# Kernel tuning notes

Hardware: AMD Instinct MI355X
Metric: run time of the kernel (lower is better)

The kernel has to match this reference:

```python
import jax, jax.numpy as jnp
import numpy as np

B, S, H, V, E = 64, 20, 128, 50257, 300


def gru(p, x, h):
    # tf.contrib.rnn.GRUCell: r,u = sigmoid([x,h]@Wg + bg); c = tanh([x, r*h]@Wc + bc); h' = u*h + (1-u)*c
    gk, gb, ck, cb = p
    xh = jnp.concatenate([x, h], axis=-1)
    r, u = jnp.split(jax.nn.sigmoid(xh @ gk + gb), 2, axis=-1)
    c = jnp.tanh(jnp.concatenate([x, r * h], axis=-1) @ ck + cb)
    return u * h + (1.0 - u) * c


def setup_inputs() -> dict:
    key = jax.random.key(0)
    ks = jax.random.split(key, 32)
    s = 0.08
    rn = lambda k, shp: (jax.random.normal(k, shp, jnp.float32) * s)
    inp = {}
    inp['x'] = jax.random.randint(ks[0], (B, S), 0, V, dtype=jnp.int32)
    inp['x_length'] = jax.random.randint(ks[1], (B,), 1, S + 1, dtype=jnp.int32)
    inp['y'] = jax.random.randint(ks[2], (B, S), 0, V, dtype=jnp.int32)
    inp['y_length'] = jax.random.randint(ks[3], (B,), 1, S + 1, dtype=jnp.int32)
    inp['embedding'] = jax.random.normal(ks[4], (V, E), jnp.float32) * 0.1
    # encoder GRU: layer0 in=E, layer1 in=H
    inp['e0_gk'] = rn(ks[5], (E + H, 2 * H)); inp['e0_gb'] = rn(ks[6], (2 * H,))
    inp['e0_ck'] = rn(ks[7], (E + H, H));     inp['e0_cb'] = rn(ks[8], (H,))
    inp['e1_gk'] = rn(ks[9], (2 * H, 2 * H)); inp['e1_gb'] = rn(ks[10], (2 * H,))
    inp['e1_ck'] = rn(ks[11], (2 * H, H));    inp['e1_cb'] = rn(ks[12], (H,))
    # decoder GRU: layer0 in = E + attention_size(H) = E+H, layer1 in=H
    inp['d0_gk'] = rn(ks[13], (E + 2 * H, 2 * H)); inp['d0_gb'] = rn(ks[14], (2 * H,))
    inp['d0_ck'] = rn(ks[15], (E + 2 * H, H));     inp['d0_cb'] = rn(ks[16], (H,))
    inp['d1_gk'] = rn(ks[17], (2 * H, 2 * H));     inp['d1_gb'] = rn(ks[18], (2 * H,))
    inp['d1_ck'] = rn(ks[19], (2 * H, H));         inp['d1_cb'] = rn(ks[20], (H,))
    # Bahdanau attention (num_units=H) + attention output layer + vocab projection
    inp['W_mem'] = rn(ks[21], (H, H))
    inp['W_q'] = rn(ks[22], (H, H))
    inp['v_att'] = rn(ks[23], (H,))
    inp['W_attn'] = rn(ks[24], (2 * H, H))
    inp['W_proj'] = rn(ks[25], (H, V))
    inp['b_proj'] = jnp.zeros((V,), jnp.float32)
    return inp


def _forward(x, x_length, y, y_length, embedding,
             e0_gk, e0_gb, e0_ck, e0_cb, e1_gk, e1_gb, e1_ck, e1_cb,
             d0_gk, d0_gb, d0_ck, d0_cb, d1_gk, d1_gb, d1_ck, d1_cb,
             W_mem, W_q, v_att, W_attn, W_proj, b_proj):
    e0 = (e0_gk, e0_gb, e0_ck, e0_cb)
    e1 = (e1_gk, e1_gb, e1_ck, e1_cb)
    d0 = (d0_gk, d0_gb, d0_ck, d0_cb)
    d1 = (d1_gk, d1_gb, d1_ck, d1_cb)
    t_idx = jnp.arange(S)
    x_valid = t_idx[None, :] < x_length[:, None]   # [B,S]
    y_valid = t_idx[None, :] < y_length[:, None]   # [B,S]

    # ---- encoder: 2-layer GRU dynamic_rnn with sequence_length semantics ----
    ex = embedding[x]                               # [B,S,E]
    zeros = jnp.zeros((x.shape[0], H), embedding.dtype)

    def enc_step(carry, inp_t):
        h0, h1 = carry
        xt, vt = inp_t                              # xt [B,E], vt [B,1]
        n0 = gru(e0, xt, h0)
        n1 = gru(e1, n0, h1)
        n0 = jnp.where(vt, n0, h0)                  # copy-through past seq end
        n1 = jnp.where(vt, n1, h1)
        return (n0, n1), jnp.where(vt, n1, 0.0)     # outputs zeroed past seq end

    (h0f, h1f), mem = jax.lax.scan(
        enc_step, (zeros, zeros),
        (ex.transpose(1, 0, 2), x_valid.T[:, :, None]))
    memory = mem.transpose(1, 0, 2)                 # [B,S,H] encoder outputs

    # ---- Bahdanau attention precompute ----
    keys = jnp.einsum('bsh,hu->bsu', memory, W_mem)  # memory_layer(memory)
    neg_inf = jnp.finfo(memory.dtype).min

    # ---- attention decoder (TrainingHelper) ----
    ey = embedding[y]                               # [B,S,E]
    attn0 = jnp.zeros((x.shape[0], H), embedding.dtype)

    def dec_step(carry, inp_t):
        h0, h1, attn = carry
        yt, vt = inp_t                              # yt [B,E], vt [B,1]
        ci = jnp.concatenate([yt, attn], axis=-1)   # cell input = [emb, prev attention]
        n0 = gru(d0, ci, h0)
        n1 = gru(d1, n0, h1)
        q = n1 @ W_q                                # query_layer(cell_output)
        sc = jnp.einsum('bsu,u->bs', jnp.tanh(keys + q[:, None, :]), v_att)
        sc = jnp.where(x_valid, sc, neg_inf)        # memory_sequence_length mask
        al = jax.nn.softmax(sc, axis=-1)            # [B,S]
        ctx = jnp.einsum('bs,bsh->bh', al, memory)  # context
        na = jnp.concatenate([n1, ctx], axis=-1) @ W_attn  # attention_layer (no bias)
        logits = na @ W_proj + b_proj               # projection_layer
        logits = jnp.where(vt, logits, 0.0)         # dynamic_decode zeroes finished emits
        return (n0, n1, na), logits

    _, logits = jax.lax.scan(
        dec_step, (h0f, h1f, attn0),
        (ey.transpose(1, 0, 2), y_valid.T[:, :, None]))
    return logits.transpose(1, 0, 2)                # [B,S,V] rnn_output


def reference(x, x_length, y, y_length, embedding,
              e0_gk, e0_gb, e0_ck, e0_cb, e1_gk, e1_gb, e1_ck, e1_cb,
              d0_gk, d0_gb, d0_ck, d0_cb, d1_gk, d1_gb, d1_ck, d1_cb,
              W_mem, W_q, v_att, W_attn, W_proj, b_proj):
    return _forward(x, x_length, y, y_length, embedding,
                    e0_gk, e0_gb, e0_ck, e0_cb, e1_gk, e1_gb, e1_ck, e1_cb,
                    d0_gk, d0_gb, d0_ck, d0_cb, d1_gk, d1_gb, d1_ck, d1_cb,
                    W_mem, W_q, v_att, W_attn, W_proj, b_proj)
```

## Files before the change

kernel.cpp:

```cpp
#include <hip/hip_runtime.h>
#include <hip/hip_bf16.h>

#define Bb 64
#define Ss 20
#define Hh 128
#define Vv 50257
#define Ee 300
#define Vpad 50304

typedef short bf16x8 __attribute__((ext_vector_type(8)));
typedef float f32x4 __attribute__((ext_vector_type(4)));

__device__ __forceinline__ unsigned short f2bf(float f){
  unsigned u = __float_as_uint(f);
  u += 0x7fff + ((u >> 16) & 1);
  return (unsigned short)(u >> 16);
}
__device__ __forceinline__ float sigm(float x){ return 1.f / (1.f + __expf(-x)); }
__device__ __forceinline__ float tanh_fast(float x){
  float e = __expf(2.f * x);
  return 1.f - 2.f / (e + 1.f);
}

template<int K4>
__device__ __forceinline__ float dotT(const float* __restrict__ w, const float* v){
  float a0 = 0.f, a1 = 0.f, a2 = 0.f, a3 = 0.f;
  const float4* w4 = (const float4*)w;
  const float4* v4 = (const float4*)v;
#pragma unroll
  for (int i = 0; i < K4; i++){
    float4 wv = w4[i]; float4 xv = v4[i];
    a0 = fmaf(wv.x, xv.x, a0); a1 = fmaf(wv.y, xv.y, a1);
    a2 = fmaf(wv.z, xv.z, a2); a3 = fmaf(wv.w, xv.w, a3);
  }
  return (a0 + a1) + (a2 + a3);
}


struct TMat { const float* src; float* dst; int r0, R, C; };
struct TList { TMat m[15]; };

__global__ __launch_bounds__(256) void wtrans_kernel(TList L){
  TMat t = L.m[blockIdx.y];
  int idx = blockIdx.x * 256 + threadIdx.x;
  int total = t.R * t.C;
  if (idx >= total) return;
  int o = idx / t.R;
  int i = idx - o * t.R;
  t.dst[idx] = t.src[(size_t)(t.r0 + i) * t.C + o];
}

__global__ __launch_bounds__(256) void wpt_kernel(const float* __restrict__ Wp,
                                                  unsigned short* __restrict__ Wpt){
  __shared__ unsigned short tile[64][136];
  int n0 = blockIdx.x * 64;
  int tid = threadIdx.x;
  for (int idx = tid; idx < 8192; idx += 256){
    int k = idx >> 6, nn = idx & 63;
    int n = n0 + nn;
    float f = (n < Vv) ? Wp[(size_t)k * Vv + n] : 0.f;
    tile[nn][k] = f2bf(f);
  }
  __syncthreads();
  for (int idx = tid; idx < 1024; idx += 256){
    int nn = idx >> 4, c = idx & 15;
    uint4 v = *reinterpret_cast<const uint4*>(&tile[nn][c * 8]);
    *reinterpret_cast<uint4*>(Wpt + (((size_t)(n0 + nn)) << 7) + c * 8) = v;
  }
}


__global__ __launch_bounds__(256) void pre_kernel(
    const int* __restrict__ x, const int* __restrict__ y, const float* __restrict__ emb,
    const float* __restrict__ egx, const float* __restrict__ ecx,
    const float* __restrict__ egb, const float* __restrict__ ecb,
    const float* __restrict__ dgx, const float* __restrict__ dcx,
    const float* __restrict__ dgb, const float* __restrict__ dcb,
    float* __restrict__ epg, float* __restrict__ epc,
    float* __restrict__ dpg, float* __restrict__ dpc)
{
  __shared__ __align__(16) float er[Ee];
  int tid = threadIdx.x, ti = blockIdx.x, which = blockIdx.y;
  int tok = which ? y[ti] : x[ti];
  if (tid < 75)
    ((float4*)er)[tid] = ((const float4*)(emb + (size_t)tok * Ee))[tid];
  __syncthreads();
  const float* gx = which ? dgx : egx;
  const float* cx = which ? dcx : ecx;
  float accg = (which ? dgb : egb)[tid] + dotT<75>(gx + (size_t)tid * Ee, er);
  (which ? dpg : epg)[ti * 256 + tid] = accg;
  if (tid < 128){
    float accc = (which ? dcb : ecb)[tid] + dotT<75>(cx + (size_t)tid * Ee, er);
    (which ? dpc : epc)[ti * 128 + tid] = accc;
  }
}


__global__ __launch_bounds__(256, 1) void recur2(
    const int* __restrict__ xlen,
    const float* __restrict__ epg, const float* __restrict__ epc,
    const float* __restrict__ dpg, const float* __restrict__ dpc,
    const float* __restrict__ e0_gh_t, const float* __restrict__ e0_ch_t,
    const float* __restrict__ e1_g_t, const float* __restrict__ e1_c_t,
    const float* __restrict__ e1_gb,  const float* __restrict__ e1_cb,
    const float* __restrict__ d0_gah_t, const float* __restrict__ d0_cah_t,
    const float* __restrict__ d1_g_t, const float* __restrict__ d1_c_t,
    const float* __restrict__ d1_gb,  const float* __restrict__ d1_cb,
    const float* __restrict__ W_mem_t, const float* __restrict__ W_q_t,
    const float* __restrict__ W_attn_t, const float* __restrict__ v_att,
    unsigned short* __restrict__ na_bf)
{
  __shared__ __align__(16) float mem_s[Ss][Hh];
  __shared__ __align__(16) float keys_s[Ss][132];
  __shared__ __align__(16) float h0[Hh], h1[Hh], attn[Hh], n0[Hh], n1[Hh], rh[Hh], q[Hh], ctx[Hh];
  __shared__ __align__(16) float gates[2*Hh];
  __shared__ __align__(16) float vatt_s[Hh];
  __shared__ float part[Ss][8], als[Ss];

  const int tid = threadIdx.x, b = blockIdx.x;
  if (tid < Hh){ h0[tid] = 0.f; h1[tid] = 0.f; attn[tid] = 0.f; vatt_s[tid] = v_att[tid]; }
  __syncthreads();
  const int xl = xlen[b];

  for (int t = 0; t < Ss; t++){
    const int tix = b * Ss + t;
    {
      float g = epg[(tix << 8) + tid] + dotT<32>(e0_gh_t + tid * 128, h0);
      float sg = sigm(g);
      if (tid < Hh) rh[tid] = sg * h0[tid];
      else          gates[tid] = sg;
    }
    __syncthreads();
    {
      int o = tid >> 1, half = tid & 1;
      float a = dotT<16>(e0_ch_t + o * 128 + half * 64, rh + half * 64);
      a += __shfl_xor(a, 1);
      if (!half){
        float c = tanh_fast(epc[(tix << 7) + o] + a);
        float u = gates[128 + o];
        n0[o] = u * h0[o] + (1.f - u) * c;
      }
    }
    __syncthreads();
    {
      float g1 = e1_gb[tid] + dotT<32>(e1_g_t + tid * 256, n0)
                            + dotT<32>(e1_g_t + tid * 256 + 128, h1);
      float sg = sigm(g1);
      if (tid < Hh) rh[tid] = sg * h1[tid];
      else          gates[tid] = sg;
    }
    __syncthreads();
    {
      int o = tid >> 1, half = tid & 1;
      const float* base = e1_c_t + o * 256 + half * 128;
      float a = half ? dotT<32>(base, rh) : dotT<32>(base, n0);
      a += __shfl_xor(a, 1);
      if (!half){
        float c = tanh_fast(e1_cb[o] + a);
        float u = gates[128 + o];
        float nh = u * h1[o] + (1.f - u) * c;
        bool v = (t < xl);
        mem_s[t][o] = v ? nh : 0.f;
        h1[o] = v ? nh : h1[o];
        h0[o] = v ? n0[o] : h0[o];
      }
    }
    __syncthreads();
  }

  for (int idx = tid; idx < Ss * Hh; idx += 256){
    int s = idx >> 7, j = idx & 127;
    keys_s[s][j] = dotT<32>(W_mem_t + j * 128, mem_s[s]);
  }
  __syncthreads();

  for (int t = 0; t < Ss; t++){
    const int tix = b * Ss + t;
    {
      float g = dpg[(tix << 8) + tid] + dotT<32>(d0_gah_t + tid * 256, attn)
                                      + dotT<32>(d0_gah_t + tid * 256 + 128, h0);
      float sg = sigm(g);
      if (tid < Hh) rh[tid] = sg * h0[tid];
      else          gates[tid] = sg;
    }
    __syncthreads();
    {
      int o = tid >> 1, half = tid & 1;
      const float* base = d0_cah_t + o * 256 + half * 128;
      float a = half ? dotT<32>(base, rh) : dotT<32>(base, attn);
      a += __shfl_xor(a, 1);
      if (!half){
        float c = tanh_fast(dpc[(tix << 7) + o] + a);
        float u = gates[128 + o];
        float nv = u * h0[o] + (1.f - u) * c;
        n0[o] = nv; h0[o] = nv;
      }
    }
    __syncthreads();
    {
      float g1 = d1_gb[tid] + dotT<32>(d1_g_t + tid * 256, n0)
                            + dotT<32>(d1_g_t + tid * 256 + 128, h1);
      float sg = sigm(g1);
      if (tid < Hh) rh[tid] = sg * h1[tid];
      else          gates[tid] = sg;
    }
    __syncthreads();
    {
      int o = tid >> 1, half = tid & 1;
      const float* base = d1_c_t + o * 256 + half * 128;
      float a = half ? dotT<32>(base, rh) : dotT<32>(base, n0);
      a += __shfl_xor(a, 1);
      if (!half){
        float c = tanh_fast(d1_cb[o] + a);
        float u = gates[128 + o];
        float nh = u * h1[o] + (1.f - u) * c;
        n1[o] = nh; h1[o] = nh;
      }
    }
    __syncthreads();
    {
      int o = tid >> 1, half = tid & 1;
      float a = dotT<16>(W_q_t + o * 128 + half * 64, n1 + half * 64);
      a += __shfl_xor(a, 1);
      if (!half) q[o] = a;
    }
    __syncthreads();
    if (tid < Ss * 8){
      int s = tid >> 3, p = tid & 7;
      float a = 0.f;
#pragma unroll
      for (int c2 = 0; c2 < 16; c2++){
        int u2 = p * 16 + c2;
        a += tanh_fast(keys_s[s][u2] + q[u2]) * vatt_s[u2];
      }
      part[s][p] = a;
    }
    __syncthreads();
    if (tid < 64){
      int s = tid;
      bool valid = (s < Ss) && (s < xl);
      float sc = -3.4e38f;
      if (valid){ sc = 0.f;
#pragma unroll
        for (int p = 0; p < 8; p++) sc += part[s][p];
      }
      float mx = sc;
#pragma unroll
      for (int off = 32; off >= 1; off >>= 1) mx = fmaxf(mx, __shfl_xor(mx, off));
      float e = valid ? __expf(sc - mx) : 0.f;
      float sm = e;
#pragma unroll
      for (int off = 32; off >= 1; off >>= 1) sm += __shfl_xor(sm, off);
      if (s < Ss) als[s] = e / sm;
    }
    __syncthreads();
    if (tid < Hh){
      float a = 0.f;
#pragma unroll
      for (int s = 0; s < Ss; s++) a += als[s] * mem_s[s][tid];
      ctx[tid] = a;
    }
    __syncthreads();
    {
      int o = tid >> 1, half = tid & 1;
      const float* base = W_attn_t + o * 256 + half * 128;
      float a = half ? dotT<32>(base, ctx) : dotT<32>(base, n1);
      a += __shfl_xor(a, 1);
      if (!half){
        attn[o] = a;
        na_bf[(tix << 7) + o] = f2bf(a);
      }
    }
    __syncthreads();
  }
}


__global__ __launch_bounds__(256) void proj2(
    const unsigned short* __restrict__ na_bf, const unsigned short* __restrict__ Wpt,
    const float* __restrict__ b_proj, const int* __restrict__ ylen,
    float* __restrict__ out)
{
  __shared__ int yl_s[Bb];
  const int tid = threadIdx.x;
  if (tid < Bb) yl_s[tid] = ylen[tid];
  const int n0 = blockIdx.x * 128, m0 = blockIdx.y * 64;
  const int lane = tid & 63, w = tid >> 6, lm = lane & 15, qq = lane >> 4;

  f32x4 acc[4][2];
#pragma unroll
  for (int mt = 0; mt < 4; mt++){ acc[mt][0] = (f32x4){0,0,0,0}; acc[mt][1] = (f32x4){0,0,0,0}; }

#pragma unroll
  for (int ks = 0; ks < 4; ks++){
    int ko = ks * 32 + qq * 8;
    bf16x8 b0 = *(const bf16x8*)(Wpt + (((size_t)(n0 + w*32 + lm)) << 7) + ko);
    bf16x8 b1 = *(const bf16x8*)(Wpt + (((size_t)(n0 + w*32 + 16 + lm)) << 7) + ko);
#pragma unroll
    for (int mt = 0; mt < 4; mt++){
      bf16x8 a = *(const bf16x8*)(na_bf + (((size_t)(m0 + mt*16 + lm)) << 7) + ko);
      acc[mt][0] = __builtin_amdgcn_mfma_f32_16x16x32_bf16(a, b0, acc[mt][0], 0, 0, 0);
      acc[mt][1] = __builtin_amdgcn_mfma_f32_16x16x32_bf16(a, b1, acc[mt][1], 0, 0, 0);
    }
  }
  __syncthreads();

#pragma unroll
  for (int mt = 0; mt < 4; mt++){
    int row = m0 + mt*16 + qq*4;
#pragma unroll
    for (int n2 = 0; n2 < 2; n2++){
      int col = n0 + w*32 + n2*16 + lm;
      if (col < Vv){
        float bp = b_proj[col];
#pragma unroll
        for (int r = 0; r < 4; r++){
          int rr = row + r;
          int bb = rr / Ss;
          int tt = rr - bb * Ss;
          float val = (tt < yl_s[bb]) ? (acc[mt][n2][r] + bp) : 0.f;
          out[(size_t)rr * Vv + col] = val;
        }
      }
    }
  }
}

extern "C" void kernel_launch(void* const* d_in, const int* in_sizes, int n_in,
                              void* d_out, int out_size, void* d_ws, size_t ws_size,
                              hipStream_t stream) {
  const int*   x        = (const int*)d_in[0];
  const int*   x_length = (const int*)d_in[1];
  const int*   y        = (const int*)d_in[2];
  const int*   y_length = (const int*)d_in[3];
  const float* emb      = (const float*)d_in[4];
  const float* e0_gk = (const float*)d_in[5];  const float* e0_gb = (const float*)d_in[6];
  const float* e0_ck = (const float*)d_in[7];  const float* e0_cb = (const float*)d_in[8];
  const float* e1_gk = (const float*)d_in[9];  const float* e1_gb = (const float*)d_in[10];
  const float* e1_ck = (const float*)d_in[11]; const float* e1_cb = (const float*)d_in[12];
  const float* d0_gk = (const float*)d_in[13]; const float* d0_gb = (const float*)d_in[14];
  const float* d0_ck = (const float*)d_in[15]; const float* d0_cb = (const float*)d_in[16];
  const float* d1_gk = (const float*)d_in[17]; const float* d1_gb = (const float*)d_in[18];
  const float* d1_ck = (const float*)d_in[19]; const float* d1_cb = (const float*)d_in[20];
  const float* W_mem = (const float*)d_in[21]; const float* W_q   = (const float*)d_in[22];
  const float* v_att = (const float*)d_in[23]; const float* W_attn= (const float*)d_in[24];
  const float* W_proj= (const float*)d_in[25]; const float* b_proj= (const float*)d_in[26];
  float* out = (float*)d_out;

  size_t off = 0;
  auto alloc = [&](size_t bytes) -> void* {
    void* p = (char*)d_ws + off;
    off += (bytes + 255) & ~(size_t)255;
    return p;
  };
  unsigned short* Wpt   = (unsigned short*)alloc((size_t)Vpad * 128 * 2);
  unsigned short* na_bf = (unsigned short*)alloc((size_t)Bb * Ss * Hh * 2);
  float* epg = (float*)alloc((size_t)Bb*Ss*256*4);
  float* epc = (float*)alloc((size_t)Bb*Ss*128*4);
  float* dpg = (float*)alloc((size_t)Bb*Ss*256*4);
  float* dpc = (float*)alloc((size_t)Bb*Ss*128*4);
  float* e0_gx_t  = (float*)alloc(256*300*4);
  float* e0_gh_t  = (float*)alloc(256*128*4);
  float* e0_cx_t  = (float*)alloc(128*300*4);
  float* e0_ch_t  = (float*)alloc(128*128*4);
  float* e1_g_t   = (float*)alloc(256*256*4);
  float* e1_c_t   = (float*)alloc(128*256*4);
  float* d0_gx_t  = (float*)alloc(256*300*4);
  float* d0_gah_t = (float*)alloc(256*256*4);
  float* d0_cx_t  = (float*)alloc(128*300*4);
  float* d0_cah_t = (float*)alloc(128*256*4);
  float* d1_g_t   = (float*)alloc(256*256*4);
  float* d1_c_t   = (float*)alloc(128*256*4);
  float* W_mem_t  = (float*)alloc(128*128*4);
  float* W_q_t    = (float*)alloc(128*128*4);
  float* W_attn_t = (float*)alloc(128*256*4);

  TList L;
  L.m[0]  = { e0_gk, e0_gx_t,    0, 300, 256 };
  L.m[1]  = { e0_gk, e0_gh_t,  300, 128, 256 };
  L.m[2]  = { e0_ck, e0_cx_t,    0, 300, 128 };
  L.m[3]  = { e0_ck, e0_ch_t,  300, 128, 128 };
  L.m[4]  = { e1_gk, e1_g_t,     0, 256, 256 };
  L.m[5]  = { e1_ck, e1_c_t,     0, 256, 128 };
  L.m[6]  = { d0_gk, d0_gx_t,    0, 300, 256 };
  L.m[7]  = { d0_gk, d0_gah_t, 300, 256, 256 };
  L.m[8]  = { d0_ck, d0_cx_t,    0, 300, 128 };
  L.m[9]  = { d0_ck, d0_cah_t, 300, 256, 128 };
  L.m[10] = { d1_gk, d1_g_t,     0, 256, 256 };
  L.m[11] = { d1_ck, d1_c_t,     0, 256, 128 };
  L.m[12] = { W_mem, W_mem_t,    0, 128, 128 };
  L.m[13] = { W_q,   W_q_t,      0, 128, 128 };
  L.m[14] = { W_attn,W_attn_t,   0, 256, 128 };

  wtrans_kernel<<<dim3(300, 15), 256, 0, stream>>>(L);
  wpt_kernel<<<Vpad / 64, 256, 0, stream>>>(W_proj, Wpt);
  pre_kernel<<<dim3(Bb * Ss, 2), 256, 0, stream>>>(
      x, y, emb, e0_gx_t, e0_cx_t, e0_gb, e0_cb,
      d0_gx_t, d0_cx_t, d0_gb, d0_cb, epg, epc, dpg, dpc);
  recur2<<<Bb, 256, 0, stream>>>(
      x_length, epg, epc, dpg, dpc,
      e0_gh_t, e0_ch_t, e1_g_t, e1_c_t, e1_gb, e1_cb,
      d0_gah_t, d0_cah_t, d1_g_t, d1_c_t, d1_gb, d1_cb,
      W_mem_t, W_q_t, W_attn_t, v_att, na_bf);
  proj2<<<dim3(Vpad / 128, (Bb * Ss) / 64), 256, 0, stream>>>(
      na_bf, Wpt, b_proj, y_length, out);
}
```

Baseline: 1.331 ms.

## Process two batch rows per recurrent block to reuse weight loads

The recurrent kernel now handles two batch elements per block, and each weight load feeds dot products for both hidden states through a new dual-vector dot helper. This halves global and L2 weight traffic per sequence, which dominates the latency-bound serial recurrence. The cost is twice the arithmetic per thread per step, larger shared memory, and only 32 blocks on a GPU with many CUs, so the serial chain per block grows longer.

```diff
diff --git a/kernel.cpp b/kernel.cpp
--- a/kernel.cpp
+++ b/kernel.cpp
@@ -34,6 +34,26 @@
     a2 = fmaf(wv.z, xv.z, a2); a3 = fmaf(wv.w, xv.w, a3);
   }
   return (a0 + a1) + (a2 + a3);
+}
+
+template<int K4>
+__device__ __forceinline__ float2 dotT2(const float* __restrict__ w,
+                                        const float* va, const float* vb){
+  float a0=0.f,a1=0.f,a2=0.f,a3=0.f, b0=0.f,b1=0.f,b2=0.f,b3=0.f;
+  const float4* w4 = (const float4*)w;
+  const float4* A4 = (const float4*)va;
+  const float4* B4 = (const float4*)vb;
+#pragma unroll
+  for (int i = 0; i < K4; i++){
+    float4 wv = w4[i];
+    float4 xa = A4[i];
+    float4 xb = B4[i];
+    a0 = fmaf(wv.x, xa.x, a0); a1 = fmaf(wv.y, xa.y, a1);
+    a2 = fmaf(wv.z, xa.z, a2); a3 = fmaf(wv.w, xa.w, a3);
+    b0 = fmaf(wv.x, xb.x, b0); b1 = fmaf(wv.y, xb.y, b1);
+    b2 = fmaf(wv.z, xb.z, b2); b3 = fmaf(wv.w, xb.w, b3);
+  }
+  return make_float2((a0 + a1) + (a2 + a3), (b0 + b1) + (b2 + b3));
 }
 
 
@@ -110,139 +130,172 @@
     const float* __restrict__ W_attn_t, const float* __restrict__ v_att,
     unsigned short* __restrict__ na_bf)
 {
-  __shared__ __align__(16) float mem_s[Ss][Hh];
-  __shared__ __align__(16) float keys_s[Ss][132];
-  __shared__ __align__(16) float h0[Hh], h1[Hh], attn[Hh], n0[Hh], n1[Hh], rh[Hh], q[Hh], ctx[Hh];
-  __shared__ __align__(16) float gates[2*Hh];
+  __shared__ __align__(16) float mem_s[2][Ss][Hh];
+  __shared__ __align__(16) float keys_s[2][Ss][132];
+  __shared__ __align__(16) float h0[2][Hh], h1[2][Hh], attn[2][Hh], n0[2][Hh], n1[2][Hh];
+  __shared__ __align__(16) float rh[2][Hh], q[2][Hh], ctx[2][Hh];
+  __shared__ __align__(16) float gates[2][2*Hh];
   __shared__ __align__(16) float vatt_s[Hh];
-  __shared__ float part[Ss][8], als[Ss];
-
-  const int tid = threadIdx.x, b = blockIdx.x;
-  if (tid < Hh){ h0[tid] = 0.f; h1[tid] = 0.f; attn[tid] = 0.f; vatt_s[tid] = v_att[tid]; }
+  __shared__ float part[2][Ss][8], als[2][Ss];
+
+  const int tid = threadIdx.x;
+  const int b0 = blockIdx.x * 2, b1 = b0 + 1;
+  if (tid < Hh){
+    h0[0][tid] = 0.f; h0[1][tid] = 0.f;
+    h1[0][tid] = 0.f; h1[1][tid] = 0.f;
+    attn[0][tid] = 0.f; attn[1][tid] = 0.f;
+    vatt_s[tid] = v_att[tid];
+  }
   __syncthreads();
-  const int xl = xlen[b];
+  const int xl0 = xlen[b0], xl1 = xlen[b1];
+  const int o = tid >> 1, half = tid & 1;
 
   for (int t = 0; t < Ss; t++){
-    const int tix = b * Ss + t;
-    {
-      float g = epg[(tix << 8) + tid] + dotT<32>(e0_gh_t + tid * 128, h0);
-      float sg = sigm(g);
-      if (tid < Hh) rh[tid] = sg * h0[tid];
-      else          gates[tid] = sg;
-    }
-    __syncthreads();
-    {
-      int o = tid >> 1, half = tid & 1;
-      float a = dotT<16>(e0_ch_t + o * 128 + half * 64, rh + half * 64);
-      a += __shfl_xor(a, 1);
+    const int tix0 = b0 * Ss + t, tix1 = b1 * Ss + t;
+    {
+      float2 g = dotT2<32>(e0_gh_t + tid * 128, h0[0], h0[1]);
+      float sa = sigm(epg[(tix0 << 8) + tid] + g.x);
+      float sb = sigm(epg[(tix1 << 8) + tid] + g.y);
+      if (tid < Hh){ rh[0][tid] = sa * h0[0][tid]; rh[1][tid] = sb * h0[1][tid]; }
+      else         { gates[0][tid] = sa;           gates[1][tid] = sb; }
+    }
+    __syncthreads();
+    {
+      float2 a = dotT2<16>(e0_ch_t + o * 128 + half * 64, rh[0] + half * 64, rh[1] + half * 64);
+      a.x += __shfl_xor(a.x, 1);
+      a.y += __shfl_xor(a.y, 1);
       if (!half){
-        float c = tanh_fast(epc[(tix << 7) + o] + a);
-        float u = gates[128 + o];
-        n0[o] = u * h0[o] + (1.f - u) * c;
-      }
-    }
-    __syncthreads();
-    {
-      float g1 = e1_gb[tid] + dotT<32>(e1_g_t + tid * 256, n0)
-                            + dotT<32>(e1_g_t + tid * 256 + 128, h1);
-      float sg = sigm(g1);
-      if (tid < Hh) rh[tid] = sg * h1[tid];
-      else          gates[tid] = sg;
-    }
-    __syncthreads();
-    {
-      int o = tid >> 1, half = tid & 1;
+        float c0 = tanh_fast(epc[(tix0 << 7) + o] + a.x);
+        float c1 = tanh_fast(epc[(tix1 << 7) + o] + a.y);
+        float u0 = gates[0][128 + o], u1 = gates[1][128 + o];
+        n0[0][o] = u0 * h0[0][o] + (1.f - u0) * c0;
+        n0[1][o] = u1 * h0[1][o] + (1.f - u1) * c1;
+      }
+    }
+    __syncthreads();
+    {
+      const float* base = e1_g_t + tid * 256;
+      float2 gA = dotT2<32>(base,       n0[0], n0[1]);
+      float2 gB = dotT2<32>(base + 128, h1[0], h1[1]);
+      float sa = sigm(e1_gb[tid] + gA.x + gB.x);
+      float sb = sigm(e1_gb[tid] + gA.y + gB.y);
+      if (tid < Hh){ rh[0][tid] = sa * h1[0][tid]; rh[1][tid] = sb * h1[1][tid]; }
+      else         { gates[0][tid] = sa;           gates[1][tid] = sb; }
+    }
+    __syncthreads();
+    {
       const float* base = e1_c_t + o * 256 + half * 128;
-      float a = half ? dotT<32>(base, rh) : dotT<32>(base, n0);
-      a += __shfl_xor(a, 1);
+      float2 a = half ? dotT2<32>(base, rh[0], rh[1]) : dotT2<32>(base, n0[0], n0[1]);
+      a.x += __shfl_xor(a.x, 1);
+      a.y += __shfl_xor(a.y, 1);
       if (!half){
-        float c = tanh_fast(e1_cb[o] + a);
-        float u = gates[128 + o];
-        float nh = u * h1[o] + (1.f - u) * c;
-        bool v = (t < xl);
-        mem_s[t][o] = v ? nh : 0.f;
-        h1[o] = v ? nh : h1[o];
-        h0[o] = v ? n0[o] : h0[o];
-      }
-    }
-    __syncthreads();
-  }
-
-  for (int idx = tid; idx < Ss * Hh; idx += 256){
-    int s = idx >> 7, j = idx & 127;
-    keys_s[s][j] = dotT<32>(W_mem_t + j * 128, mem_s[s]);
+        float c0 = tanh_fast(e1_cb[o] + a.x);
+        float c1 = tanh_fast(e1_cb[o] + a.y);
+        float u0 = gates[0][128 + o], u1 = gates[1][128 + o];
+        float nh0 = u0 * h1[0][o] + (1.f - u0) * c0;
+        float nh1 = u1 * h1[1][o] + (1.f - u1) * c1;
+        bool v0 = (t < xl0), v1 = (t < xl1);
+        mem_s[0][t][o] = v0 ? nh0 : 0.f;
+        mem_s[1][t][o] = v1 ? nh1 : 0.f;
+        h1[0][o] = v0 ? nh0 : h1[0][o];
+        h1[1][o] = v1 ? nh1 : h1[1][o];
+        h0[0][o] = v0 ? n0[0][o] : h0[0][o];
+        h0[1][o] = v1 ? n0[1][o] : h0[1][o];
+      }
+    }
+    __syncthreads();
+  }
+
+  for (int idx = tid; idx < 2 * Ss * Hh; idx += 256){
+    int g = idx / (Ss * Hh);
+    int r = idx - g * (Ss * Hh);
+    int s = r >> 7, j = r & 127;
+    keys_s[g][s][j] = dotT<32>(W_mem_t + j * 128, mem_s[g][s]);
   }
   __syncthreads();
 
   for (int t = 0; t < Ss; t++){
-    const int tix = b * Ss + t;
-    {
-      float g = dpg[(tix << 8) + tid] + dotT<32>(d0_gah_t + tid * 256, attn)
-                                      + dotT<32>(d0_gah_t + tid * 256 + 128, h0);
-      float sg = sigm(g);
-      if (tid < Hh) rh[tid] = sg * h0[tid];
-      else          gates[tid] = sg;
-    }
-    __syncthreads();
-    {
-      int o = tid >> 1, half = tid & 1;
+    const int tix0 = b0 * Ss + t, tix1 = b1 * Ss + t;
+    {
+      const float* base = d0_gah_t + tid * 256;
+      float2 gA = dotT2<32>(base,       attn[0], attn[1]);
+      float2 gB = dotT2<32>(base + 128, h0[0],   h0[1]);
+      float sa = sigm(dpg[(tix0 << 8) + tid] + gA.x + gB.x);
+      float sb = sigm(dpg[(tix1 << 8) + tid] + gA.y + gB.y);
+      if (tid < Hh){ rh[0][tid] = sa * h0[0][tid]; rh[1][tid] = sb * h0[1][tid]; }
+      else         { gates[0][tid] = sa;           gates[1][tid] = sb; }
+    }
+    __syncthreads();
+    {
       const float* base = d0_cah_t + o * 256 + half * 128;
-      float a = half ? dotT<32>(base, rh) : dotT<32>(base, attn);
-      a += __shfl_xor(a, 1);
+      float2 a = half ? dotT2<32>(base, rh[0], rh[1]) : dotT2<32>(base, attn[0], attn[1]);
+      a.x += __shfl_xor(a.x, 1);
+      a.y += __shfl_xor(a.y, 1);
       if (!half){
-        float c = tanh_fast(dpc[(tix << 7) + o] + a);
-        float u = gates[128 + o];
-        float nv = u * h0[o] + (1.f - u) * c;
-        n0[o] = nv; h0[o] = nv;
-      }
-    }
-    __syncthreads();
-    {
-      float g1 = d1_gb[tid] + dotT<32>(d1_g_t + tid * 256, n0)
-                            + dotT<32>(d1_g_t + tid * 256 + 128, h1);
-      float sg = sigm(g1);
-      if (tid < Hh) rh[tid] = sg * h1[tid];
-      else          gates[tid] = sg;
-    }
-    __syncthreads();
-    {
-      int o = tid >> 1, half = tid & 1;
+        float c0 = tanh_fast(dpc[(tix0 << 7) + o] + a.x);
+        float c1 = tanh_fast(dpc[(tix1 << 7) + o] + a.y);
+        float u0 = gates[0][128 + o], u1 = gates[1][128 + o];
+        float nv0 = u0 * h0[0][o] + (1.f - u0) * c0;
+        float nv1 = u1 * h0[1][o] + (1.f - u1) * c1;
+        n0[0][o] = nv0; h0[0][o] = nv0;
+        n0[1][o] = nv1; h0[1][o] = nv1;
+      }
+    }
+    __syncthreads();
+    {
+      const float* base = d1_g_t + tid * 256;
+      float2 gA = dotT2<32>(base,       n0[0], n0[1]);
+      float2 gB = dotT2<32>(base + 128, h1[0], h1[1]);
+      float sa = sigm(d1_gb[tid] + gA.x + gB.x);
+      float sb = sigm(d1_gb[tid] + gA.y + gB.y);
+      if (tid < Hh){ rh[0][tid] = sa * h1[0][tid]; rh[1][tid] = sb * h1[1][tid]; }
+      else         { gates[0][tid] = sa;           gates[1][tid] = sb; }
+    }
+    __syncthreads();
+    {
       const float* base = d1_c_t + o * 256 + half * 128;
-      float a = half ? dotT<32>(base, rh) : dotT<32>(base, n0);
-      a += __shfl_xor(a, 1);
+      float2 a = half ? dotT2<32>(base, rh[0], rh[1]) : dotT2<32>(base, n0[0], n0[1]);
+      a.x += __shfl_xor(a.x, 1);
+      a.y += __shfl_xor(a.y, 1);
       if (!half){
-        float c = tanh_fast(d1_cb[o] + a);
-        float u = gates[128 + o];
-        float nh = u * h1[o] + (1.f - u) * c;
-        n1[o] = nh; h1[o] = nh;
-      }
-    }
-    __syncthreads();
-    {
-      int o = tid >> 1, half = tid & 1;
-      float a = dotT<16>(W_q_t + o * 128 + half * 64, n1 + half * 64);
-      a += __shfl_xor(a, 1);
-      if (!half) q[o] = a;
-    }
-    __syncthreads();
-    if (tid < Ss * 8){
-      int s = tid >> 3, p = tid & 7;
+        float c0 = tanh_fast(d1_cb[o] + a.x);
+        float c1 = tanh_fast(d1_cb[o] + a.y);
+        float u0 = gates[0][128 + o], u1 = gates[1][128 + o];
+        float nh0 = u0 * h1[0][o] + (1.f - u0) * c0;
+        float nh1 = u1 * h1[1][o] + (1.f - u1) * c1;
+        n1[0][o] = nh0; h1[0][o] = nh0;
+        n1[1][o] = nh1; h1[1][o] = nh1;
+      }
+    }
+    __syncthreads();
+    {
+      float2 a = dotT2<16>(W_q_t + o * 128 + half * 64, n1[0] + half * 64, n1[1] + half * 64);
+      a.x += __shfl_xor(a.x, 1);
+      a.y += __shfl_xor(a.y, 1);
+      if (!half){ q[0][o] = a.x; q[1][o] = a.y; }
+    }
+    __syncthreads();
+    for (int idx = tid; idx < 2 * Ss * 8; idx += 256){
+      int g = idx / 160;
+      int r = idx - g * 160;
+      int s = r >> 3, p = r & 7;
       float a = 0.f;
 #pragma unroll
       for (int c2 = 0; c2 < 16; c2++){
         int u2 = p * 16 + c2;
-        a += tanh_fast(keys_s[s][u2] + q[u2]) * vatt_s[u2];
-      }
-      part[s][p] = a;
-    }
-    __syncthreads();
-    if (tid < 64){
-      int s = tid;
-      bool valid = (s < Ss) && (s < xl);
+        a += tanh_fast(keys_s[g][s][u2] + q[g][u2]) * vatt_s[u2];
+      }
+      part[g][s][p] = a;
+    }
+    __syncthreads();
+    if (tid < 128){
+      int g = tid >> 6, s = tid & 63;
+      int xlg = g ? xl1 : xl0;
+      bool valid = (s < Ss) && (s < xlg);
       float sc = -3.4e38f;
       if (valid){ sc = 0.f;
 #pragma unroll
-        for (int p = 0; p < 8; p++) sc += part[s][p];
+        for (int p = 0; p < 8; p++) sc += part[g][s][p];
       }
       float mx = sc;
 #pragma unroll
@@ -251,24 +304,25 @@
       float sm = e;
 #pragma unroll
       for (int off = 32; off >= 1; off >>= 1) sm += __shfl_xor(sm, off);
-      if (s < Ss) als[s] = e / sm;
-    }
-    __syncthreads();
-    if (tid < Hh){
+      if (s < Ss) als[g][s] = e / sm;
+    }
+    __syncthreads();
+    {
+      int g = tid >> 7, col = tid & 127;
       float a = 0.f;
 #pragma unroll
-      for (int s = 0; s < Ss; s++) a += als[s] * mem_s[s][tid];
-      ctx[tid] = a;
-    }
-    __syncthreads();
-    {
-      int o = tid >> 1, half = tid & 1;
+      for (int s = 0; s < Ss; s++) a = fmaf(als[g][s], mem_s[g][s][col], a);
+      ctx[g][col] = a;
+    }
+    __syncthreads();
+    {
       const float* base = W_attn_t + o * 256 + half * 128;
-      float a = half ? dotT<32>(base, ctx) : dotT<32>(base, n1);
-      a += __shfl_xor(a, 1);
+      float2 a = half ? dotT2<32>(base, ctx[0], ctx[1]) : dotT2<32>(base, n1[0], n1[1]);
+      a.x += __shfl_xor(a.x, 1);
+      a.y += __shfl_xor(a.y, 1);
       if (!half){
-        attn[o] = a;
-        na_bf[(tix << 7) + o] = f2bf(a);
+        attn[0][o] = a.x;  na_bf[(tix0 << 7) + o] = f2bf(a.x);
+        attn[1][o] = a.y;  na_bf[(tix1 << 7) + o] = f2bf(a.y);
       }
     }
     __syncthreads();
@@ -397,7 +451,7 @@
   pre_kernel<<<dim3(Bb * Ss, 2), 256, 0, stream>>>(
       x, y, emb, e0_gx_t, e0_cx_t, e0_gb, e0_cb,
       d0_gx_t, d0_cx_t, d0_gb, d0_cb, epg, epc, dpg, dpc);
-  recur2<<<Bb, 256, 0, stream>>>(
+  recur2<<<Bb / 2, 256, 0, stream>>>(
       x_length, epg, epc, dpg, dpc,
       e0_gh_t, e0_ch_t, e1_g_t, e1_c_t, e1_gb, e1_cb,
       d0_gah_t, d0_cah_t, d1_g_t, d1_c_t, d1_gb, d1_cb,
```

Measured after the change: 1.666 ms. +25.2%, slower.
